# Kernel optimization log

Measured on AMD Instinct MI355X. Metric: run time of the kernel, lower is better.

The kernel has to match this reference:

```python
import jax, jax.numpy as jnp
import numpy as np

H = 4096
EPS = 1e-5


def _ln(x, g, b):
    # LayerNorm over last dim
    m = jnp.mean(x, axis=-1, keepdims=True)
    v = jnp.var(x, axis=-1, keepdims=True)
    return (x - m) * jax.lax.rsqrt(v + EPS) * g + b


def setup_inputs() -> dict:
    key = jax.random.key(0)
    ks = jax.random.split(key, 5)
    scale = 1.0 / np.sqrt(2 * H)  # ~ torch Linear init scale
    return {
        "h0": jax.random.normal(ks[0], (H,), dtype=jnp.float32),
        "c0": jax.random.normal(ks[1], (H,), dtype=jnp.float32),
        "h1": jax.random.normal(ks[2], (H,), dtype=jnp.float32),
        "c1": jax.random.normal(ks[3], (H,), dtype=jnp.float32),
        "W": jax.random.normal(ks[4], (5 * H, 2 * H), dtype=jnp.float32) * scale,
        "ffio_g": jnp.ones((4, H), dtype=jnp.float32),
        "ffio_b": jnp.zeros((4, H), dtype=jnp.float32),
        "u_g": jnp.ones((H,), dtype=jnp.float32),
        "u_b": jnp.zeros((H,), dtype=jnp.float32),
        "c_g": jnp.ones((H,), dtype=jnp.float32),
        "c_b": jnp.zeros((H,), dtype=jnp.float32),
    }


def reference(h0, c0, h1, c1, W, ffio_g, ffio_b, u_g, u_b, c_g, c_b):
    h = h0.shape[0]
    # ffiou_linear (no bias): [2H] @ [2H,5H] -> [5H], split into 5 chunks of [H]
    z = jnp.concatenate([h0, h1], axis=0) @ W.T
    parts = z.reshape(5, h)
    # f0, f1, i, o gates: per-gate LayerNorm then sigmoid (vectorized over the 4 gates)
    f0, f1, i, o = jax.nn.sigmoid(_ln(parts[:4], ffio_g, ffio_b))
    # u: LayerNorm then tanh (dropout=0 -> identity)
    u = jnp.tanh(_ln(parts[4], u_g, u_b))
    new_cell = _ln(i * u + f0 * c0 + f1 * c1, c_g, c_b)
    new_hidden = o * jnp.tanh(new_cell)
    return (new_hidden, new_cell)
```

## Files before the change

### kernel.cpp

```cpp
#include <hip/hip_runtime.h>
#include <math.h>

#define H 4096
#define TWO_H 8192
#define FIVE_H 20480
#define EPS 1e-5f

__global__ __launch_bounds__(256) void matvec_kernel(
    const float* __restrict__ W, const float* __restrict__ h0,
    const float* __restrict__ h1, float* __restrict__ z) {
  const int row0 = blockIdx.x * 4;
  const int tid = threadIdx.x;

  float4 xv[8];
  const float4* x0 = (const float4*)h0;
  const float4* x1 = (const float4*)h1;
#pragma unroll
  for (int j = 0; j < 4; ++j) xv[j] = x0[j * 256 + tid];
#pragma unroll
  for (int j = 0; j < 4; ++j) xv[4 + j] = x1[j * 256 + tid];

  float acc[4] = {0.f, 0.f, 0.f, 0.f};
#pragma unroll
  for (int r = 0; r < 4; ++r) {
    const float4* Wrow = (const float4*)(W + (size_t)(row0 + r) * TWO_H);
#pragma unroll
    for (int j = 0; j < 8; ++j) {
      float4 w = Wrow[j * 256 + tid];
      acc[r] += w.x * xv[j].x + w.y * xv[j].y + w.z * xv[j].z + w.w * xv[j].w;
    }
  }

  __shared__ float red[4][4];
  const int lane = tid & 63;
  const int wv = tid >> 6;
#pragma unroll
  for (int r = 0; r < 4; ++r) {
    float a = acc[r];
#pragma unroll
    for (int off = 32; off; off >>= 1) a += __shfl_down(a, off, 64);
    if (lane == 0) red[wv][r] = a;
  }
  __syncthreads();
  if (tid < 4) {
    z[row0 + tid] = red[0][tid] + red[1][tid] + red[2][tid] + red[3][tid];
  }
}

__device__ __forceinline__ float block_sum_1024(float v, float* sred) {
#pragma unroll
  for (int off = 32; off; off >>= 1) v += __shfl_down(v, off, 64);
  const int lane = threadIdx.x & 63;
  const int wv = threadIdx.x >> 6;
  __syncthreads();
  if (lane == 0) sred[wv] = v;
  __syncthreads();
  float s = 0.f;
#pragma unroll
  for (int w = 0; w < 16; ++w) s += sred[w];
  return s;
}

__global__ __launch_bounds__(1024) void epilogue_kernel(
    const float* __restrict__ z, const float* __restrict__ c0,
    const float* __restrict__ c1, const float* __restrict__ ffio_g,
    const float* __restrict__ ffio_b, const float* __restrict__ u_g,
    const float* __restrict__ u_b, const float* __restrict__ c_g,
    const float* __restrict__ c_b, float* __restrict__ out) {
  const int tid = threadIdx.x;
  __shared__ float sred[16];

  float zp[5][4];
#pragma unroll
  for (int p = 0; p < 5; ++p)
#pragma unroll
    for (int j = 0; j < 4; ++j) zp[p][j] = z[p * H + j * 1024 + tid];

  float mean[5], rstd[5];
#pragma unroll
  for (int p = 0; p < 5; ++p) {
    float s = zp[p][0] + zp[p][1] + zp[p][2] + zp[p][3];
    float q = zp[p][0] * zp[p][0] + zp[p][1] * zp[p][1] +
              zp[p][2] * zp[p][2] + zp[p][3] * zp[p][3];
    s = block_sum_1024(s, sred);
    q = block_sum_1024(q, sred);
    float m = s * (1.0f / H);
    float v = q * (1.0f / H) - m * m;
    mean[p] = m;
    rstd[p] = rsqrtf(v + EPS);
  }

  float oo[4], cpre[4];
#pragma unroll
  for (int j = 0; j < 4; ++j) {
    const int e = tid + j * 1024;
    float n0 = (zp[0][j] - mean[0]) * rstd[0] * ffio_g[0 * H + e] + ffio_b[0 * H + e];
    float n1 = (zp[1][j] - mean[1]) * rstd[1] * ffio_g[1 * H + e] + ffio_b[1 * H + e];
    float n2 = (zp[2][j] - mean[2]) * rstd[2] * ffio_g[2 * H + e] + ffio_b[2 * H + e];
    float n3 = (zp[3][j] - mean[3]) * rstd[3] * ffio_g[3 * H + e] + ffio_b[3 * H + e];
    float n4 = (zp[4][j] - mean[4]) * rstd[4] * u_g[e] + u_b[e];
    float f0 = 1.f / (1.f + expf(-n0));
    float f1 = 1.f / (1.f + expf(-n1));
    float ig = 1.f / (1.f + expf(-n2));
    oo[j]    = 1.f / (1.f + expf(-n3));
    float uu = tanhf(n4);
    cpre[j] = ig * uu + f0 * c0[e] + f1 * c1[e];
  }

  {
    float s = cpre[0] + cpre[1] + cpre[2] + cpre[3];
    float q = cpre[0] * cpre[0] + cpre[1] * cpre[1] + cpre[2] * cpre[2] +
              cpre[3] * cpre[3];
    s = block_sum_1024(s, sred);
    q = block_sum_1024(q, sred);
    float m = s * (1.0f / H);
    float v = q * (1.0f / H) - m * m;
    float r = rsqrtf(v + EPS);
#pragma unroll
    for (int j = 0; j < 4; ++j) {
      const int e = tid + j * 1024;
      float ncell = (cpre[j] - m) * r * c_g[e] + c_b[e];
      out[H + e] = ncell;
      out[e] = oo[j] * tanhf(ncell);
    }
  }
}

extern "C" void kernel_launch(void* const* d_in, const int* in_sizes, int n_in,
                              void* d_out, int out_size, void* d_ws,
                              size_t ws_size, hipStream_t stream) {
  const float* h0 = (const float*)d_in[0];
  const float* c0 = (const float*)d_in[1];
  const float* h1 = (const float*)d_in[2];
  const float* c1 = (const float*)d_in[3];
  const float* W = (const float*)d_in[4];
  const float* ffio_g = (const float*)d_in[5];
  const float* ffio_b = (const float*)d_in[6];
  const float* u_g = (const float*)d_in[7];
  const float* u_b = (const float*)d_in[8];
  const float* c_g = (const float*)d_in[9];
  const float* c_b = (const float*)d_in[10];
  float* out = (float*)d_out;
  float* z = (float*)d_ws;

  matvec_kernel<<<FIVE_H / 4, 256, 0, stream>>>(W, h0, h1, z);
  epilogue_kernel<<<1, 1024, 0, stream>>>(z, c0, c1, ffio_g, ffio_b, u_g, u_b,
                                          c_g, c_b, out);
}
```

Before: 852.6 us.

## Assign two rows per wavefront in matvec, use nontemporal loads, batch epilogue reductions

The matvec now gives each 64-lane wavefront two full rows of W instead of splitting rows across the whole block. This removes the shared-memory cross-wave reduction and the __syncthreads, and W is streamed with nontemporal loads so it does not pollute the cache. The grid is halved to 2560 blocks of 8 rows. The epilogue vectorizes its loads and stores and merges the ten LayerNorm sums into one block reduction instead of ten sequential ones. The trade-off is fewer independent loads in flight per wave, and the x vector is now reloaded per iteration rather than kept in registers.

```diff
diff --git a/kernel.cpp b/kernel.cpp
--- a/kernel.cpp
+++ b/kernel.cpp
@@ -6,59 +6,52 @@
 #define FIVE_H 20480
 #define EPS 1e-5f
 
+typedef float v4f __attribute__((ext_vector_type(4)));
+
 __global__ __launch_bounds__(256) void matvec_kernel(
     const float* __restrict__ W, const float* __restrict__ h0,
     const float* __restrict__ h1, float* __restrict__ z) {
-  const int row0 = blockIdx.x * 4;
   const int tid = threadIdx.x;
+  const int lane = tid & 63;
+  const int wv = tid >> 6;
+  const int row0 = blockIdx.x * 8 + wv * 2;
 
-  float4 xv[8];
-  const float4* x0 = (const float4*)h0;
-  const float4* x1 = (const float4*)h1;
-#pragma unroll
-  for (int j = 0; j < 4; ++j) xv[j] = x0[j * 256 + tid];
-#pragma unroll
-  for (int j = 0; j < 4; ++j) xv[4 + j] = x1[j * 256 + tid];
+  const v4f* __restrict__ Wa = (const v4f*)(W + (size_t)row0 * TWO_H);
+  const v4f* __restrict__ Wb = Wa + (TWO_H / 4);
+  const v4f* __restrict__ x0 = (const v4f*)h0;
+  const v4f* __restrict__ x1 = (const v4f*)h1;
 
-  float acc[4] = {0.f, 0.f, 0.f, 0.f};
-#pragma unroll
-  for (int r = 0; r < 4; ++r) {
-    const float4* Wrow = (const float4*)(W + (size_t)(row0 + r) * TWO_H);
-#pragma unroll
-    for (int j = 0; j < 8; ++j) {
-      float4 w = Wrow[j * 256 + tid];
-      acc[r] += w.x * xv[j].x + w.y * xv[j].y + w.z * xv[j].z + w.w * xv[j].w;
-    }
+  float acc0 = 0.f, acc1 = 0.f;
+
+#pragma unroll 4
+  for (int i = 0; i < 16; ++i) {
+    const int idx = i * 64 + lane;
+    v4f xv = x0[idx];
+    v4f wa = __builtin_nontemporal_load(&Wa[idx]);
+    v4f wb = __builtin_nontemporal_load(&Wb[idx]);
+    acc0 += wa[0] * xv[0] + wa[1] * xv[1] + wa[2] * xv[2] + wa[3] * xv[3];
+    acc1 += wb[0] * xv[0] + wb[1] * xv[1] + wb[2] * xv[2] + wb[3] * xv[3];
+  }
+#pragma unroll 4
+  for (int i = 0; i < 16; ++i) {
+    const int idx = i * 64 + lane;
+    const int widx = idx + 1024;
+    v4f xv = x1[idx];
+    v4f wa = __builtin_nontemporal_load(&Wa[widx]);
+    v4f wb = __builtin_nontemporal_load(&Wb[widx]);
+    acc0 += wa[0] * xv[0] + wa[1] * xv[1] + wa[2] * xv[2] + wa[3] * xv[3];
+    acc1 += wb[0] * xv[0] + wb[1] * xv[1] + wb[2] * xv[2] + wb[3] * xv[3];
   }
 
-  __shared__ float red[4][4];
-  const int lane = tid & 63;
-  const int wv = tid >> 6;
 #pragma unroll
-  for (int r = 0; r < 4; ++r) {
-    float a = acc[r];
-#pragma unroll
-    for (int off = 32; off; off >>= 1) a += __shfl_down(a, off, 64);
-    if (lane == 0) red[wv][r] = a;
+  for (int off = 32; off; off >>= 1) {
+    acc0 += __shfl_down(acc0, off, 64);
+    acc1 += __shfl_down(acc1, off, 64);
   }
-  __syncthreads();
-  if (tid < 4) {
-    z[row0 + tid] = red[0][tid] + red[1][tid] + red[2][tid] + red[3][tid];
+  if (lane == 0) {
+    z[row0] = acc0;
+    z[row0 + 1] = acc1;
   }
-}
-
-__device__ __forceinline__ float block_sum_1024(float v, float* sred) {
-#pragma unroll
-  for (int off = 32; off; off >>= 1) v += __shfl_down(v, off, 64);
-  const int lane = threadIdx.x & 63;
-  const int wv = threadIdx.x >> 6;
-  __syncthreads();
-  if (lane == 0) sred[wv] = v;
-  __syncthreads();
-  float s = 0.f;
-#pragma unroll
-  for (int w = 0; w < 16; ++w) s += sred[w];
-  return s;
 }
 
 __global__ __launch_bounds__(1024) void epilogue_kernel(
@@ -68,61 +61,110 @@
     const float* __restrict__ u_b, const float* __restrict__ c_g,
     const float* __restrict__ c_b, float* __restrict__ out) {
   const int tid = threadIdx.x;
-  __shared__ float sred[16];
+  const int lane = tid & 63;
+  const int wv = tid >> 6;
 
-  float zp[5][4];
+  __shared__ float sredA[10][16];
+  __shared__ float sredB[2][16];
+
+  const v4f* __restrict__ z4 = (const v4f*)z;
+
+  v4f zp[5];
+  float vals[10];
 #pragma unroll
-  for (int p = 0; p < 5; ++p)
+  for (int p = 0; p < 5; ++p) {
+    zp[p] = z4[p * (H / 4) + tid];
+    vals[2 * p] = zp[p][0] + zp[p][1] + zp[p][2] + zp[p][3];
+    vals[2 * p + 1] = zp[p][0] * zp[p][0] + zp[p][1] * zp[p][1] +
+                      zp[p][2] * zp[p][2] + zp[p][3] * zp[p][3];
+  }
+
 #pragma unroll
-    for (int j = 0; j < 4; ++j) zp[p][j] = z[p * H + j * 1024 + tid];
+  for (int off = 32; off; off >>= 1)
+#pragma unroll
+    for (int k = 0; k < 10; ++k) vals[k] += __shfl_down(vals[k], off, 64);
+  if (lane == 0)
+#pragma unroll
+    for (int k = 0; k < 10; ++k) sredA[k][wv] = vals[k];
+  __syncthreads();
 
   float mean[5], rstd[5];
 #pragma unroll
   for (int p = 0; p < 5; ++p) {
-    float s = zp[p][0] + zp[p][1] + zp[p][2] + zp[p][3];
-    float q = zp[p][0] * zp[p][0] + zp[p][1] * zp[p][1] +
-              zp[p][2] * zp[p][2] + zp[p][3] * zp[p][3];
-    s = block_sum_1024(s, sred);
-    q = block_sum_1024(q, sred);
+    float s = 0.f, q = 0.f;
+#pragma unroll
+    for (int w = 0; w < 16; ++w) {
+      s += sredA[2 * p][w];
+      q += sredA[2 * p + 1][w];
+    }
     float m = s * (1.0f / H);
     float v = q * (1.0f / H) - m * m;
     mean[p] = m;
     rstd[p] = rsqrtf(v + EPS);
   }
 
-  float oo[4], cpre[4];
+  v4f gg[4], gb[4];
+#pragma unroll
+  for (int p = 0; p < 4; ++p) {
+    gg[p] = ((const v4f*)ffio_g)[p * (H / 4) + tid];
+    gb[p] = ((const v4f*)ffio_b)[p * (H / 4) + tid];
+  }
+  v4f ug = ((const v4f*)u_g)[tid];
+  v4f ub = ((const v4f*)u_b)[tid];
+  v4f c0v = ((const v4f*)c0)[tid];
+  v4f c1v = ((const v4f*)c1)[tid];
+
+  v4f oo, cpre;
 #pragma unroll
   for (int j = 0; j < 4; ++j) {
-    const int e = tid + j * 1024;
-    float n0 = (zp[0][j] - mean[0]) * rstd[0] * ffio_g[0 * H + e] + ffio_b[0 * H + e];
-    float n1 = (zp[1][j] - mean[1]) * rstd[1] * ffio_g[1 * H + e] + ffio_b[1 * H + e];
-    float n2 = (zp[2][j] - mean[2]) * rstd[2] * ffio_g[2 * H + e] + ffio_b[2 * H + e];
-    float n3 = (zp[3][j] - mean[3]) * rstd[3] * ffio_g[3 * H + e] + ffio_b[3 * H + e];
-    float n4 = (zp[4][j] - mean[4]) * rstd[4] * u_g[e] + u_b[e];
+    float n0 = (zp[0][j] - mean[0]) * rstd[0] * gg[0][j] + gb[0][j];
+    float n1 = (zp[1][j] - mean[1]) * rstd[1] * gg[1][j] + gb[1][j];
+    float n2 = (zp[2][j] - mean[2]) * rstd[2] * gg[2][j] + gb[2][j];
+    float n3 = (zp[3][j] - mean[3]) * rstd[3] * gg[3][j] + gb[3][j];
+    float n4 = (zp[4][j] - mean[4]) * rstd[4] * ug[j] + ub[j];
     float f0 = 1.f / (1.f + expf(-n0));
     float f1 = 1.f / (1.f + expf(-n1));
     float ig = 1.f / (1.f + expf(-n2));
-    oo[j]    = 1.f / (1.f + expf(-n3));
+    oo[j] = 1.f / (1.f + expf(-n3));
     float uu = tanhf(n4);
-    cpre[j] = ig * uu + f0 * c0[e] + f1 * c1[e];
+    cpre[j] = ig * uu + f0 * c0v[j] + f1 * c1v[j];
   }
 
   {
     float s = cpre[0] + cpre[1] + cpre[2] + cpre[3];
     float q = cpre[0] * cpre[0] + cpre[1] * cpre[1] + cpre[2] * cpre[2] +
               cpre[3] * cpre[3];
-    s = block_sum_1024(s, sred);
-    q = block_sum_1024(q, sred);
+#pragma unroll
+    for (int off = 32; off; off >>= 1) {
+      s += __shfl_down(s, off, 64);
+      q += __shfl_down(q, off, 64);
+    }
+    if (lane == 0) {
+      sredB[0][wv] = s;
+      sredB[1][wv] = q;
+    }
+    __syncthreads();
+    s = 0.f;
+    q = 0.f;
+#pragma unroll
+    for (int w = 0; w < 16; ++w) {
+      s += sredB[0][w];
+      q += sredB[1][w];
+    }
     float m = s * (1.0f / H);
     float v = q * (1.0f / H) - m * m;
     float r = rsqrtf(v + EPS);
+
+    v4f cgv = ((const v4f*)c_g)[tid];
+    v4f cbv = ((const v4f*)c_b)[tid];
+    v4f cell, hid;
 #pragma unroll
     for (int j = 0; j < 4; ++j) {
-      const int e = tid + j * 1024;
-      float ncell = (cpre[j] - m) * r * c_g[e] + c_b[e];
-      out[H + e] = ncell;
-      out[e] = oo[j] * tanhf(ncell);
+      cell[j] = (cpre[j] - m) * r * cgv[j] + cbv[j];
+      hid[j] = oo[j] * tanhf(cell[j]);
     }
+    ((v4f*)out)[(H / 4) + tid] = cell;
+    ((v4f*)out)[tid] = hid;
   }
 }
 
@@ -143,7 +185,7 @@
   float* out = (float*)d_out;
   float* z = (float*)d_ws;
 
-  matvec_kernel<<<FIVE_H / 4, 256, 0, stream>>>(W, h0, h1, z);
+  matvec_kernel<<<FIVE_H / 8, 256, 0, stream>>>(W, h0, h1, z);
   epilogue_kernel<<<1, 1024, 0, stream>>>(z, c0, c1, ffio_g, ffio_b, u_g, u_b,
                                           c_g, c_b, out);
 }
```

After: 853.0 us. No clear change (+0.0%).
